# Kernel tuning notes

Measured on AMD Instinct MI355X. Metric: run time of the kernel, lower is better.

The kernel has to match this reference:

```python
import jax, jax.numpy as jnp
import numpy as np

S, N, M, D = 4, 4096, 4096, 128
NEG = -1e30
EPS = 1e-12


def setup_inputs() -> dict:
    key = jax.random.key(0)
    k1, k2, k3 = jax.random.split(key, 3)
    art = jax.random.normal(k1, (S, N, D), dtype=jnp.float32)
    ref = jax.random.normal(k2, (S, M, D), dtype=jnp.float32)
    pos_mask = jax.random.randint(k3, (S, N, M), 0, 2).astype(jnp.bool_)
    log_temperature = jnp.log(jnp.asarray(0.01, dtype=jnp.float32))
    return {"art": art, "ref": ref, "pos_mask": pos_mask, "log_temperature": log_temperature}


def _l2norm(x):
    # F.normalize: x / max(||x||, eps)
    n = jnp.sqrt(jnp.sum(x * x, axis=-1, keepdims=True))
    return x / jnp.maximum(n, EPS)


def reference(art, ref, pos_mask, log_temperature):
    temp = jnp.exp(log_temperature)
    a = _l2norm(art)                                   # [S,N,D]
    r = _l2norm(ref)                                   # [S,M,D]
    logits = jnp.einsum("snd,smd->snm", a, r) / temp   # [S,N,M]

    den = jax.nn.logsumexp(logits, axis=-1)                              # [S,N]
    num = jax.nn.logsumexp(jnp.where(pos_mask, logits, NEG), axis=-1)    # [S,N]

    n_pos = jnp.sum(pos_mask, axis=-1)                 # [S,N]
    n_ref = logits.shape[-1]
    valid = (n_pos > 0) & (n_ref > n_pos)              # skip anchors with 0 pos or all pos

    per_anchor = den - num                             # -(num - den)
    cnt = jnp.sum(valid, axis=-1)                      # [S]
    stem_loss = jnp.sum(jnp.where(valid, per_anchor, 0.0), axis=-1) / jnp.maximum(cnt, 1)
    stem_valid = cnt > 0
    loss = jnp.sum(jnp.where(stem_valid, stem_loss, 0.0)) / jnp.maximum(jnp.sum(stem_valid), 1)
    return loss
```

## Files before the change

kernel.cpp:

```cpp
#include <hip/hip_runtime.h>
#include <hip/hip_bf16.h>
#include <math.h>

#define S_ 4
#define N_ 4096
#define M_ 4096
#define D_ 128
#define NEG_ (-1e30f)
#define CH_ 2
#define MCH_ (M_ / CH_)
#define NST_ (MCH_ / 64)
#define NGRP_ (NST_ / 4)
#define LN2_ 0.69314718055994531f
#define LOG2E_ 1.44269504088896340f

typedef __bf16 bf16x8 __attribute__((ext_vector_type(8)));
typedef float f32x4 __attribute__((ext_vector_type(4)));

__device__ __forceinline__ void gll16(const void* g, void* l) {
    __builtin_amdgcn_global_load_lds(
        (const __attribute__((address_space(1))) unsigned int*)g,
        (__attribute__((address_space(3))) unsigned int*)l, 16, 0, 0);
}

__device__ __forceinline__ unsigned short f2bf(float f) {
    unsigned u = __float_as_uint(f);
    unsigned r = (u + 0x7FFFu + ((u >> 16) & 1u)) >> 16;
    return (unsigned short)r;
}

__global__ void nrm_rows_kernel(const float* __restrict__ art, const float* __restrict__ ref,
                                unsigned short* __restrict__ an, unsigned short* __restrict__ rn) {
    const int w = threadIdx.x >> 6;
    const int lane = threadIdx.x & 63;
    const int half = lane >> 5;
    const int li = lane & 31;
    const int row = blockIdx.x * 8 + w * 2 + half;
    const bool is_art = row < S_ * N_;
    const float* src = is_art ? (art + (size_t)row * D_)
                              : (ref + (size_t)(row - S_ * N_) * D_);
    unsigned short* dst = is_art ? (an + (size_t)row * D_)
                                 : (rn + (size_t)(row - S_ * N_) * D_);
    const float4 v = *reinterpret_cast<const float4*>(src + li * 4);
    float ss = v.x * v.x + v.y * v.y + v.z * v.z + v.w * v.w;
#pragma unroll
    for (int off = 1; off < 32; off <<= 1) ss += __shfl_xor(ss, off);
    const float scale = 1.0f / fmaxf(sqrtf(ss), 1e-12f);
    uint2 pack;
    pack.x = (unsigned)f2bf(v.x * scale) | ((unsigned)f2bf(v.y * scale) << 16);
    pack.y = (unsigned)f2bf(v.z * scale) | ((unsigned)f2bf(v.w * scale) << 16);
    *reinterpret_cast<uint2*>(dst + li * 4) = pack;
}

template <int ESZ>
__device__ __forceinline__ void mload(int4* mq, const unsigned char* __restrict__ maskb,
                                      const size_t* rowb, int g, int lane) {
#pragma unroll
    for (int r = 0; r < 8; ++r) {
        const unsigned char* p = maskb + rowb[r] + (size_t)((g * 256 + 4 * lane) * ESZ);
        if (ESZ == 4) mq[r] = *reinterpret_cast<const int4*>(p);
        else          mq[r].x = *reinterpret_cast<const int*>(p);
    }
}

template <int ESZ>
__device__ __forceinline__ unsigned nib_of(const int4 q) {
    if (ESZ == 4)
        return (unsigned)((q.x != 0) | ((q.y != 0) << 1) | ((q.z != 0) << 2) | ((q.w != 0) << 3));
    const unsigned b = (unsigned)q.x;
    return (((b & 0xFFu) != 0) ? 1u : 0u) | (((b >> 8) & 0xFFu) ? 2u : 0u)
         | (((b >> 16) & 0xFFu) ? 4u : 0u) | ((b >> 24) ? 8u : 0u);
}

template <int ESZ>
__device__ __forceinline__ void run_main(
    const unsigned short* __restrict__ an, const unsigned short* __restrict__ rn,
    const unsigned char* __restrict__ maskb, float scale2, float4* __restrict__ part4,
    int s, int ch, int n_base,
    unsigned char (&smem)[2][64 * 256], unsigned char (&mnib)[2][32][68],
    float4 (&lds4)[4][16]) {

    const int tid = threadIdx.x;
    const int w = tid >> 6;
    const int lane = tid & 63;
    const int nsub = w & 1;
    const int msub = w >> 1;
    const int n16 = n_base + nsub * 16;
    const int lrow = lane & 15;
    const int lgrp = lane >> 4;

    bf16x8 bfr[4];
    const unsigned short* abase = an + ((size_t)(s * N_ + n16 + lrow)) * D_ + lgrp * 8;
#pragma unroll
    for (int kc = 0; kc < 4; ++kc)
        bfr[kc] = *reinterpret_cast<const bf16x8*>(abase + kc * 32);

    const int srow = w * 4 + (lane >> 4);
    const int schunk = (lane & 15) ^ (srow & 7);
    const int lane_src_off = srow * 256 + schunk * 16;
    const unsigned char* rn_chunk =
        (const unsigned char*)(rn + ((size_t)(s * M_ + ch * MCH_)) * D_);

    size_t rowb[8];
#pragma unroll
    for (int r = 0; r < 8; ++r)
        rowb[r] = ((size_t)(s * N_ + n_base + w * 8 + r) * M_ + (size_t)ch * MCH_) * ESZ;

    const int rb0 = (msub * 32 + lrow) * 256;
    int coff[4];
#pragma unroll
    for (int kc = 0; kc < 4; ++kc) coff[kc] = ((kc * 4 + lgrp) ^ (lrow & 7)) * 16;

    float dmax = NEG_, dsum = 0.f, nsum = 0.f;
    int npos = 0;
    int4 mq[8];

    {
        const unsigned char* src = rn_chunk + lane_src_off;
        unsigned char* dst = &smem[0][w * 1024];
#pragma unroll
        for (int j = 0; j < 4; ++j) gll16(src + j * 4096, dst + j * 4096);
        mload<ESZ>(mq, maskb, rowb, 0, lane);
#pragma unroll
        for (int r = 0; r < 8; ++r)
            mnib[0][w * 8 + r][lane] = (unsigned char)nib_of<ESZ>(mq[r]);
        mload<ESZ>(mq, maskb, rowb, 1, lane);
        __syncthreads();
    }

    for (int g = 0; g < NGRP_; ++g) {
#pragma unroll
        for (int j = 0; j < 4; ++j) {
            const int st = g * 4 + j;
            const int nb = j & 1;
            if (j < 3 || g < NGRP_ - 1) {
                const unsigned char* src_ = rn_chunk + (size_t)(st + 1) * 16384 + lane_src_off;
                unsigned char* dst_ = &smem[nb ^ 1][w * 1024];
#pragma unroll
                for (int jj = 0; jj < 4; ++jj) gll16(src_ + jj * 4096, dst_ + jj * 4096);
            }
            if (j == 3 && g < NGRP_ - 1) {
#pragma unroll
                for (int r = 0; r < 8; ++r)
                    mnib[(g + 1) & 1][w * 8 + r][lane] = (unsigned char)nib_of<ESZ>(mq[r]);
                if (g < NGRP_ - 2) mload<ESZ>(mq, maskb, rowb, g + 2, lane);
            }
            const unsigned char* base_ = &smem[nb][0] + rb0;
            f32x4 acc0 = {0.f, 0.f, 0.f, 0.f}, acc1 = {0.f, 0.f, 0.f, 0.f};
#pragma unroll
            for (int kc = 0; kc < 4; ++kc) {
                acc0 = __builtin_amdgcn_mfma_f32_16x16x32_bf16(
                    *reinterpret_cast<const bf16x8*>(base_ + coff[kc]), bfr[kc], acc0, 0, 0, 0);
                acc1 = __builtin_amdgcn_mfma_f32_16x16x32_bf16(
                    *reinterpret_cast<const bf16x8*>(base_ + 4096 + coff[kc]), bfr[kc], acc1, 0, 0, 0);
            }
            const int row = nsub * 16 + lrow;
            const int nidx = j * 16 + msub * 8 + lgrp;
            const unsigned nib0 = mnib[g & 1][row][nidx];
            const unsigned nib1 = mnib[g & 1][row][nidx + 4];
            float l0 = acc0[0] * scale2, l1 = acc0[1] * scale2;
            float l2 = acc0[2] * scale2, l3 = acc0[3] * scale2;
            float l4 = acc1[0] * scale2, l5 = acc1[1] * scale2;
            float l6 = acc1[2] * scale2, l7 = acc1[3] * scale2;
            float tmax = fmaxf(fmaxf(fmaxf(l0, l1), fmaxf(l2, l3)),
                               fmaxf(fmaxf(l4, l5), fmaxf(l6, l7)));
            const float nmx = fmaxf(dmax, tmax);
            const float r_ = exp2f(dmax - nmx);
            float e0 = exp2f(l0 - nmx), e1 = exp2f(l1 - nmx);
            float e2 = exp2f(l2 - nmx), e3 = exp2f(l3 - nmx);
            float e4 = exp2f(l4 - nmx), e5 = exp2f(l5 - nmx);
            float e6 = exp2f(l6 - nmx), e7 = exp2f(l7 - nmx);
            dsum = dsum * r_ + (((e0 + e1) + (e2 + e3)) + ((e4 + e5) + (e6 + e7)));
            float p0 = ((nib0 & 1u) ? e0 : 0.f) + (((nib0 >> 1) & 1u) ? e1 : 0.f);
            float p1 = (((nib0 >> 2) & 1u) ? e2 : 0.f) + (((nib0 >> 3) & 1u) ? e3 : 0.f);
            float p2 = ((nib1 & 1u) ? e4 : 0.f) + (((nib1 >> 1) & 1u) ? e5 : 0.f);
            float p3 = (((nib1 >> 2) & 1u) ? e6 : 0.f) + (((nib1 >> 3) & 1u) ? e7 : 0.f);
            nsum = nsum * r_ + ((p0 + p1) + (p2 + p3));
            npos += __popc(nib0 | (nib1 << 4));
            dmax = nmx;
            __syncthreads();
        }
    }

    float npf = (float)npos;
#pragma unroll
    for (int off = 16; off < 64; off <<= 1) {
        float odm = __shfl_xor(dmax, off), ods = __shfl_xor(dsum, off);
        float ons = __shfl_xor(nsum, off), onp = __shfl_xor(npf, off);
        float nm = fmaxf(dmax, odm);
        float ra = exp2f(dmax - nm), rb = exp2f(odm - nm);
        dsum = dsum * ra + ods * rb;
        nsum = nsum * ra + ons * rb;
        npf += onp;
        dmax = nm;
    }

    if (lane < 16) lds4[w][lane] = make_float4(dmax, dsum, nsum, npf);
    __syncthreads();

    if (w == 0 && lane < 32) {
        const int wsub = lane >> 4;
        const int ni = lane & 15;
        const float4 A = lds4[wsub][ni];
        const float4 B = lds4[wsub + 2][ni];
        const float nm = fmaxf(A.x, B.x);
        const float ra = exp2f(A.x - nm), rb = exp2f(B.x - nm);
        const float ds = A.y * ra + B.y * rb;
        const float ns = A.z * ra + B.z * rb;
        const float np = A.w + B.w;
        const int ag = s * N_ + n_base + wsub * 16 + ni;
        part4[ag * CH_ + ch] = make_float4(nm, ds, ns, np);
    }
}

__global__ __launch_bounds__(256, 4) void infonce_main_kernel(
    const unsigned short* __restrict__ an, const unsigned short* __restrict__ rn,
    const unsigned char* __restrict__ maskb, const float* __restrict__ logtemp,
    float4* __restrict__ part4) {

    const int bid = blockIdx.x;
    const int swz = (bid & 7) * 128 + (bid >> 3);
    const int ch = swz >> 9;
    const int s = (swz >> 7) & 3;
    const int n_base = (swz & 127) * 32;
    const float scale2 = __expf(-logtemp[0]) * LOG2E_;

    const unsigned* mu = (const unsigned*)maskb;
    unsigned pr = 0;
#pragma unroll
    for (int i = 0; i < 4; ++i) pr |= (mu[i * 64 + (threadIdx.x & 63)] > 1u) ? 1u : 0u;
    const bool byte_mode = (__ballot(pr != 0) != 0ull);

    __shared__ unsigned char smem[2][64 * 256];
    __shared__ unsigned char mnib[2][32][68];
    __shared__ float4 lds4[4][16];

    if (byte_mode)
        run_main<1>(an, rn, maskb, scale2, part4, s, ch, n_base, smem, mnib, lds4);
    else
        run_main<4>(an, rn, maskb, scale2, part4, s, ch, n_base, smem, mnib, lds4);
}

__global__ void reduce_kernel(const float4* __restrict__ part4, float2* __restrict__ bpart) {
    const int a = blockIdx.x * 256 + threadIdx.x;
    const int w = threadIdx.x >> 6;
    const int lane = threadIdx.x & 63;
    float dm = NEG_, ds = 0.f, ns = 0.f, npf = 0.f;
#pragma unroll
    for (int ch = 0; ch < CH_; ++ch) {
        const float4 p = part4[a * CH_ + ch];
        const float m2 = fmaxf(dm, p.x);
        const float ra = exp2f(dm - m2), rb = exp2f(p.x - m2);
        ds = ds * ra + p.y * rb;
        ns = ns * ra + p.z * rb;
        npf += p.w;
        dm = m2;
    }
    const bool valid = (npf > 0.5f) && (npf < (float)M_ - 0.5f);
    float pa = valid ? LN2_ * (log2f(ds) - log2f(ns)) : 0.f;
    float cv = valid ? 1.f : 0.f;
#pragma unroll
    for (int off = 1; off < 64; off <<= 1) {
        pa += __shfl_xor(pa, off);
        cv += __shfl_xor(cv, off);
    }
    __shared__ float sp[4], sc[4];
    if (lane == 0) { sp[w] = pa; sc[w] = cv; }
    __syncthreads();
    if (threadIdx.x == 0)
        bpart[blockIdx.x] = make_float2(sp[0] + sp[1] + sp[2] + sp[3],
                                        sc[0] + sc[1] + sc[2] + sc[3]);
}

__global__ void finalize_kernel(const float2* __restrict__ bpart, float* __restrict__ out) {
    const int t = threadIdx.x;
    const float2 v = bpart[t];
    float pa = v.x, cv = v.y;
#pragma unroll
    for (int off = 1; off < 16; off <<= 1) {
        pa += __shfl_xor(pa, off);
        cv += __shfl_xor(cv, off);
    }
    const float p0 = __shfl(pa, 0),  c0 = __shfl(cv, 0);
    const float p1 = __shfl(pa, 16), c1 = __shfl(cv, 16);
    const float p2 = __shfl(pa, 32), c2 = __shfl(cv, 32);
    const float p3 = __shfl(pa, 48), c3 = __shfl(cv, 48);
    if (t == 0) {
        float total = 0.f;
        int scnt = 0;
        const float ps[4] = {p0, p1, p2, p3};
        const float cs[4] = {c0, c1, c2, c3};
        for (int s = 0; s < S_; ++s) {
            const float stem = ps[s] / fmaxf(cs[s], 1.f);
            if (cs[s] > 0.f) { total += stem; scnt++; }
        }
        out[0] = total / (float)(scnt > 0 ? scnt : 1);
    }
}

extern "C" void kernel_launch(void* const* d_in, const int* in_sizes, int n_in,
                              void* d_out, int out_size, void* d_ws, size_t ws_size,
                              hipStream_t stream) {
    const float* art = (const float*)d_in[0];
    const float* ref = (const float*)d_in[1];
    const unsigned char* mask = (const unsigned char*)d_in[2];
    const float* lt = (const float*)d_in[3];
    float* out = (float*)d_out;

    char* ws = (char*)d_ws;
    unsigned short* an = (unsigned short*)ws;
    unsigned short* rn = (unsigned short*)(ws + (size_t)4194304);
    float4* part4 = (float4*)(ws + (size_t)8388608);
    float2* bpart = (float2*)(ws + (size_t)9437184);

    nrm_rows_kernel<<<(S_ * (N_ + M_)) / 8, 256, 0, stream>>>(art, ref, an, rn);
    infonce_main_kernel<<<S_ * (N_ / 32) * CH_, 256, 0, stream>>>(an, rn, mask, lt, part4);
    reduce_kernel<<<(S_ * N_) / 256, 256, 0, stream>>>(part4, bpart);
    finalize_kernel<<<1, 64, 0, stream>>>(bpart, out);
}
```

Before: 400.3 us.

## Enlarge anchor tile to 128 rows and drop online max with fixed logit shift

Each block now handles 128 anchor rows instead of 32. Each wave computes a 32x64 logit tile, so every reference tile staged in LDS is reused across four times as many anchors, and the reference range is split into 4 chunks instead of 2. The running-max softmax is replaced by a constant shift of half the logit scale, which relies on the inputs being unit-normalised so the logits stay bounded. The mask is now read as contiguous per-row words and packed into 64-bit bitmasks in LDS. This removes the per-step rescaling and the cross-wave merge, at the cost of more registers (launch bound lowered to 2) and a risk of exp overflow or underflow if the temperature changes.

```diff
diff --git a/kernel.cpp b/kernel.cpp
--- a/kernel.cpp
+++ b/kernel.cpp
@@ -6,11 +6,10 @@
 #define N_ 4096
 #define M_ 4096
 #define D_ 128
-#define NEG_ (-1e30f)
-#define CH_ 2
+#define BN_ 128
+#define CH_ 4
 #define MCH_ (M_ / CH_)
 #define NST_ (MCH_ / 64)
-#define NGRP_ (NST_ / 4)
 #define LN2_ 0.69314718055994531f
 #define LOG2E_ 1.44269504088896340f
 
@@ -52,24 +51,41 @@
     *reinterpret_cast<uint2*>(dst + li * 4) = pack;
 }
 
+__device__ __forceinline__ unsigned nib4(int a, int b, int c, int d) {
+    return (unsigned)((a != 0) | ((b != 0) << 1) | ((c != 0) << 2) | ((d != 0) << 3));
+}
+__device__ __forceinline__ unsigned nib_bytes(unsigned b) {
+    return ((b & 0xFFu) ? 1u : 0u) | ((b & 0xFF00u) ? 2u : 0u)
+         | ((b & 0xFF0000u) ? 4u : 0u) | ((b & 0xFF000000u) ? 8u : 0u);
+}
+
 template <int ESZ>
-__device__ __forceinline__ void mload(int4* mq, const unsigned char* __restrict__ maskb,
-                                      const size_t* rowb, int g, int lane) {
-#pragma unroll
-    for (int r = 0; r < 8; ++r) {
-        const unsigned char* p = maskb + rowb[r] + (size_t)((g * 256 + 4 * lane) * ESZ);
-        if (ESZ == 4) mq[r] = *reinterpret_cast<const int4*>(p);
-        else          mq[r].x = *reinterpret_cast<const int*>(p);
-    }
-}
-
+__device__ __forceinline__ void mload(int4* mq, const unsigned char* p) {
+    if (ESZ == 4) {
+#pragma unroll
+        for (int j = 0; j < 8; ++j) mq[j] = *reinterpret_cast<const int4*>(p + j * 16);
+    } else {
+        mq[0] = *reinterpret_cast<const int4*>(p);
+        mq[1] = *reinterpret_cast<const int4*>(p + 16);
+    }
+}
 template <int ESZ>
-__device__ __forceinline__ unsigned nib_of(const int4 q) {
-    if (ESZ == 4)
-        return (unsigned)((q.x != 0) | ((q.y != 0) << 1) | ((q.z != 0) << 2) | ((q.w != 0) << 3));
-    const unsigned b = (unsigned)q.x;
-    return (((b & 0xFFu) != 0) ? 1u : 0u) | (((b >> 8) & 0xFFu) ? 2u : 0u)
-         | (((b >> 16) & 0xFFu) ? 4u : 0u) | ((b >> 24) ? 8u : 0u);
+__device__ __forceinline__ unsigned mconv(const int4* mq) {
+    unsigned u = 0;
+    if (ESZ == 4) {
+#pragma unroll
+        for (int j = 0; j < 8; ++j)
+            u |= nib4(mq[j].x, mq[j].y, mq[j].z, mq[j].w) << (4 * j);
+    } else {
+#pragma unroll
+        for (int k = 0; k < 2; ++k) {
+            u |= nib_bytes((unsigned)mq[k].x) << ((k * 4 + 0) * 4);
+            u |= nib_bytes((unsigned)mq[k].y) << ((k * 4 + 1) * 4);
+            u |= nib_bytes((unsigned)mq[k].z) << ((k * 4 + 2) * 4);
+            u |= nib_bytes((unsigned)mq[k].w) << ((k * 4 + 3) * 4);
+        }
+    }
+    return u;
 }
 
 template <int ESZ>
@@ -77,23 +93,24 @@
     const unsigned short* __restrict__ an, const unsigned short* __restrict__ rn,
     const unsigned char* __restrict__ maskb, float scale2, float4* __restrict__ part4,
     int s, int ch, int n_base,
-    unsigned char (&smem)[2][64 * 256], unsigned char (&mnib)[2][32][68],
-    float4 (&lds4)[4][16]) {
+    unsigned char (&smem)[2][64 * 256], unsigned long long (&mtab)[2][BN_]) {
 
     const int tid = threadIdx.x;
     const int w = tid >> 6;
     const int lane = tid & 63;
-    const int nsub = w & 1;
-    const int msub = w >> 1;
-    const int n16 = n_base + nsub * 16;
     const int lrow = lane & 15;
     const int lgrp = lane >> 4;
-
-    bf16x8 bfr[4];
-    const unsigned short* abase = an + ((size_t)(s * N_ + n16 + lrow)) * D_ + lgrp * 8;
-#pragma unroll
-    for (int kc = 0; kc < 4; ++kc)
-        bfr[kc] = *reinterpret_cast<const bf16x8*>(abase + kc * 32);
+    const float negC = -0.5f * scale2;
+
+    bf16x8 bfr[2][4];
+#pragma unroll
+    for (int nc = 0; nc < 2; ++nc) {
+        const unsigned short* abase =
+            an + ((size_t)(s * N_ + n_base + w * 32 + nc * 16 + lrow)) * D_ + lgrp * 8;
+#pragma unroll
+        for (int kc = 0; kc < 4; ++kc)
+            bfr[nc][kc] = *reinterpret_cast<const bf16x8*>(abase + kc * 32);
+    }
 
     const int srow = w * 4 + (lane >> 4);
     const int schunk = (lane & 15) ^ (srow & 7);
@@ -101,128 +118,100 @@
     const unsigned char* rn_chunk =
         (const unsigned char*)(rn + ((size_t)(s * M_ + ch * MCH_)) * D_);
 
-    size_t rowb[8];
-#pragma unroll
-    for (int r = 0; r < 8; ++r)
-        rowb[r] = ((size_t)(s * N_ + n_base + w * 8 + r) * M_ + (size_t)ch * MCH_) * ESZ;
-
-    const int rb0 = (msub * 32 + lrow) * 256;
-    int coff[4];
-#pragma unroll
-    for (int kc = 0; kc < 4; ++kc) coff[kc] = ((kc * 4 + lgrp) ^ (lrow & 7)) * 16;
-
-    float dmax = NEG_, dsum = 0.f, nsum = 0.f;
-    int npos = 0;
-    int4 mq[8];
+    const int mrow = w * 32 + (lane >> 1);
+    const int h = lane & 1;
+    const unsigned char* mbase = maskb +
+        ((size_t)(s * N_ + n_base + mrow) * M_ + (size_t)(ch * MCH_ + h * 32)) * ESZ;
+
+    float dsum0 = 0.f, dsum1 = 0.f, nsum0 = 0.f, nsum1 = 0.f;
+    int npos0 = 0, npos1 = 0;
+    int4 mq[ESZ == 4 ? 8 : 2];
 
     {
         const unsigned char* src = rn_chunk + lane_src_off;
         unsigned char* dst = &smem[0][w * 1024];
 #pragma unroll
         for (int j = 0; j < 4; ++j) gll16(src + j * 4096, dst + j * 4096);
-        mload<ESZ>(mq, maskb, rowb, 0, lane);
-#pragma unroll
-        for (int r = 0; r < 8; ++r)
-            mnib[0][w * 8 + r][lane] = (unsigned char)nib_of<ESZ>(mq[r]);
-        mload<ESZ>(mq, maskb, rowb, 1, lane);
+        mload<ESZ>(mq, mbase);
+        reinterpret_cast<unsigned*>(&mtab[0][mrow])[h] = mconv<ESZ>(mq);
+        mload<ESZ>(mq, mbase + (size_t)64 * ESZ);
         __syncthreads();
     }
 
-    for (int g = 0; g < NGRP_; ++g) {
-#pragma unroll
-        for (int j = 0; j < 4; ++j) {
-            const int st = g * 4 + j;
-            const int nb = j & 1;
-            if (j < 3 || g < NGRP_ - 1) {
-                const unsigned char* src_ = rn_chunk + (size_t)(st + 1) * 16384 + lane_src_off;
-                unsigned char* dst_ = &smem[nb ^ 1][w * 1024];
-#pragma unroll
-                for (int jj = 0; jj < 4; ++jj) gll16(src_ + jj * 4096, dst_ + jj * 4096);
+    for (int st = 0; st < NST_; ++st) {
+        const int buf = st & 1;
+        if (st + 1 < NST_) {
+            const unsigned char* src = rn_chunk + (size_t)(st + 1) * 16384 + lane_src_off;
+            unsigned char* dst = &smem[buf ^ 1][w * 1024];
+#pragma unroll
+            for (int j = 0; j < 4; ++j) gll16(src + j * 4096, dst + j * 4096);
+            reinterpret_cast<unsigned*>(&mtab[buf ^ 1][mrow])[h] = mconv<ESZ>(mq);
+        }
+        if (st + 2 < NST_) mload<ESZ>(mq, mbase + (size_t)(st + 2) * 64 * ESZ);
+
+        const unsigned char* base_ = &smem[buf][0];
+        f32x4 acc[4][2] = {};
+#pragma unroll
+        for (int mt = 0; mt < 4; ++mt) {
+            const int rowb = (mt * 16 + lrow) * 256;
+#pragma unroll
+            for (int kc = 0; kc < 4; ++kc) {
+                const bf16x8 af = *reinterpret_cast<const bf16x8*>(
+                    base_ + rowb + (((kc * 4 + lgrp) ^ (lrow & 7)) * 16));
+                acc[mt][0] = __builtin_amdgcn_mfma_f32_16x16x32_bf16(af, bfr[0][kc], acc[mt][0], 0, 0, 0);
+                acc[mt][1] = __builtin_amdgcn_mfma_f32_16x16x32_bf16(af, bfr[1][kc], acc[mt][1], 0, 0, 0);
             }
-            if (j == 3 && g < NGRP_ - 1) {
-#pragma unroll
-                for (int r = 0; r < 8; ++r)
-                    mnib[(g + 1) & 1][w * 8 + r][lane] = (unsigned char)nib_of<ESZ>(mq[r]);
-                if (g < NGRP_ - 2) mload<ESZ>(mq, maskb, rowb, g + 2, lane);
+        }
+        const unsigned long long w0 = mtab[buf][w * 32 + lrow];
+        const unsigned long long w1 = mtab[buf][w * 32 + 16 + lrow];
+        float d0 = 0.f, d1 = 0.f, n0 = 0.f, n1 = 0.f;
+#pragma unroll
+        for (int mt = 0; mt < 4; ++mt) {
+            const unsigned nib0 = (unsigned)(w0 >> ((mt * 4 + lgrp) * 4)) & 0xFu;
+            const unsigned nib1 = (unsigned)(w1 >> ((mt * 4 + lgrp) * 4)) & 0xFu;
+            float e0[4], e1[4];
+#pragma unroll
+            for (int i = 0; i < 4; ++i) {
+                e0[i] = exp2f(fmaf(acc[mt][0][i], scale2, negC));
+                e1[i] = exp2f(fmaf(acc[mt][1][i], scale2, negC));
             }
-            const unsigned char* base_ = &smem[nb][0] + rb0;
-            f32x4 acc0 = {0.f, 0.f, 0.f, 0.f}, acc1 = {0.f, 0.f, 0.f, 0.f};
-#pragma unroll
-            for (int kc = 0; kc < 4; ++kc) {
-                acc0 = __builtin_amdgcn_mfma_f32_16x16x32_bf16(
-                    *reinterpret_cast<const bf16x8*>(base_ + coff[kc]), bfr[kc], acc0, 0, 0, 0);
-                acc1 = __builtin_amdgcn_mfma_f32_16x16x32_bf16(
-                    *reinterpret_cast<const bf16x8*>(base_ + 4096 + coff[kc]), bfr[kc], acc1, 0, 0, 0);
-            }
-            const int row = nsub * 16 + lrow;
-            const int nidx = j * 16 + msub * 8 + lgrp;
-            const unsigned nib0 = mnib[g & 1][row][nidx];
-            const unsigned nib1 = mnib[g & 1][row][nidx + 4];
-            float l0 = acc0[0] * scale2, l1 = acc0[1] * scale2;
-            float l2 = acc0[2] * scale2, l3 = acc0[3] * scale2;
-            float l4 = acc1[0] * scale2, l5 = acc1[1] * scale2;
-            float l6 = acc1[2] * scale2, l7 = acc1[3] * scale2;
-            float tmax = fmaxf(fmaxf(fmaxf(l0, l1), fmaxf(l2, l3)),
-                               fmaxf(fmaxf(l4, l5), fmaxf(l6, l7)));
-            const float nmx = fmaxf(dmax, tmax);
-            const float r_ = exp2f(dmax - nmx);
-            float e0 = exp2f(l0 - nmx), e1 = exp2f(l1 - nmx);
-            float e2 = exp2f(l2 - nmx), e3 = exp2f(l3 - nmx);
-            float e4 = exp2f(l4 - nmx), e5 = exp2f(l5 - nmx);
-            float e6 = exp2f(l6 - nmx), e7 = exp2f(l7 - nmx);
-            dsum = dsum * r_ + (((e0 + e1) + (e2 + e3)) + ((e4 + e5) + (e6 + e7)));
-            float p0 = ((nib0 & 1u) ? e0 : 0.f) + (((nib0 >> 1) & 1u) ? e1 : 0.f);
-            float p1 = (((nib0 >> 2) & 1u) ? e2 : 0.f) + (((nib0 >> 3) & 1u) ? e3 : 0.f);
-            float p2 = ((nib1 & 1u) ? e4 : 0.f) + (((nib1 >> 1) & 1u) ? e5 : 0.f);
-            float p3 = (((nib1 >> 2) & 1u) ? e6 : 0.f) + (((nib1 >> 3) & 1u) ? e7 : 0.f);
-            nsum = nsum * r_ + ((p0 + p1) + (p2 + p3));
-            npos += __popc(nib0 | (nib1 << 4));
-            dmax = nmx;
-            __syncthreads();
-        }
-    }
-
-    float npf = (float)npos;
+            d0 += (e0[0] + e0[1]) + (e0[2] + e0[3]);
+            d1 += (e1[0] + e1[1]) + (e1[2] + e1[3]);
+            n0 += (((nib0 & 1u) ? e0[0] : 0.f) + (((nib0 >> 1) & 1u) ? e0[1] : 0.f))
+                + ((((nib0 >> 2) & 1u) ? e0[2] : 0.f) + (((nib0 >> 3) & 1u) ? e0[3] : 0.f));
+            n1 += (((nib1 & 1u) ? e1[0] : 0.f) + (((nib1 >> 1) & 1u) ? e1[1] : 0.f))
+                + ((((nib1 >> 2) & 1u) ? e1[2] : 0.f) + (((nib1 >> 3) & 1u) ? e1[3] : 0.f));
+            npos0 += __popc(nib0);
+            npos1 += __popc(nib1);
+        }
+        dsum0 += d0; dsum1 += d1; nsum0 += n0; nsum1 += n1;
+        __syncthreads();
+    }
+
+    float npf0 = (float)npos0, npf1 = (float)npos1;
 #pragma unroll
     for (int off = 16; off < 64; off <<= 1) {
-        float odm = __shfl_xor(dmax, off), ods = __shfl_xor(dsum, off);
-        float ons = __shfl_xor(nsum, off), onp = __shfl_xor(npf, off);
-        float nm = fmaxf(dmax, odm);
-        float ra = exp2f(dmax - nm), rb = exp2f(odm - nm);
-        dsum = dsum * ra + ods * rb;
-        nsum = nsum * ra + ons * rb;
-        npf += onp;
-        dmax = nm;
-    }
-
-    if (lane < 16) lds4[w][lane] = make_float4(dmax, dsum, nsum, npf);
-    __syncthreads();
-
-    if (w == 0 && lane < 32) {
-        const int wsub = lane >> 4;
-        const int ni = lane & 15;
-        const float4 A = lds4[wsub][ni];
-        const float4 B = lds4[wsub + 2][ni];
-        const float nm = fmaxf(A.x, B.x);
-        const float ra = exp2f(A.x - nm), rb = exp2f(B.x - nm);
-        const float ds = A.y * ra + B.y * rb;
-        const float ns = A.z * ra + B.z * rb;
-        const float np = A.w + B.w;
-        const int ag = s * N_ + n_base + wsub * 16 + ni;
-        part4[ag * CH_ + ch] = make_float4(nm, ds, ns, np);
-    }
-}
-
-__global__ __launch_bounds__(256, 4) void infonce_main_kernel(
+        dsum0 += __shfl_xor(dsum0, off); dsum1 += __shfl_xor(dsum1, off);
+        nsum0 += __shfl_xor(nsum0, off); nsum1 += __shfl_xor(nsum1, off);
+        npf0  += __shfl_xor(npf0, off);  npf1  += __shfl_xor(npf1, off);
+    }
+    if (lane < 16) {
+        const int ag0 = s * N_ + n_base + w * 32 + lane;
+        part4[ag0 * CH_ + ch] = make_float4(dsum0, nsum0, npf0, 0.f);
+        part4[(ag0 + 16) * CH_ + ch] = make_float4(dsum1, nsum1, npf1, 0.f);
+    }
+}
+
+__global__ __launch_bounds__(256, 2) void infonce_main_kernel(
     const unsigned short* __restrict__ an, const unsigned short* __restrict__ rn,
     const unsigned char* __restrict__ maskb, const float* __restrict__ logtemp,
     float4* __restrict__ part4) {
 
     const int bid = blockIdx.x;
-    const int swz = (bid & 7) * 128 + (bid >> 3);
-    const int ch = swz >> 9;
-    const int s = (swz >> 7) & 3;
-    const int n_base = (swz & 127) * 32;
+    const int swz = (bid & 7) * 64 + (bid >> 3);
+    const int ch = swz >> 7;
+    const int s = (swz >> 5) & 3;
+    const int n_base = (swz & 31) * BN_;
     const float scale2 = __expf(-logtemp[0]) * LOG2E_;
 
     const unsigned* mu = (const unsigned*)maskb;
@@ -232,29 +221,23 @@
     const bool byte_mode = (__ballot(pr != 0) != 0ull);
 
     __shared__ unsigned char smem[2][64 * 256];
-    __shared__ unsigned char mnib[2][32][68];
-    __shared__ float4 lds4[4][16];
+    __shared__ unsigned long long mtab[2][BN_];
 
     if (byte_mode)
-        run_main<1>(an, rn, maskb, scale2, part4, s, ch, n_base, smem, mnib, lds4);
+        run_main<1>(an, rn, maskb, scale2, part4, s, ch, n_base, smem, mtab);
     else
-        run_main<4>(an, rn, maskb, scale2, part4, s, ch, n_base, smem, mnib, lds4);
+        run_main<4>(an, rn, maskb, scale2, part4, s, ch, n_base, smem, mtab);
 }
 
 __global__ void reduce_kernel(const float4* __restrict__ part4, float2* __restrict__ bpart) {
     const int a = blockIdx.x * 256 + threadIdx.x;
     const int w = threadIdx.x >> 6;
     const int lane = threadIdx.x & 63;
-    float dm = NEG_, ds = 0.f, ns = 0.f, npf = 0.f;
+    float ds = 0.f, ns = 0.f, npf = 0.f;
 #pragma unroll
     for (int ch = 0; ch < CH_; ++ch) {
         const float4 p = part4[a * CH_ + ch];
-        const float m2 = fmaxf(dm, p.x);
-        const float ra = exp2f(dm - m2), rb = exp2f(p.x - m2);
-        ds = ds * ra + p.y * rb;
-        ns = ns * ra + p.z * rb;
-        npf += p.w;
-        dm = m2;
+        ds += p.x; ns += p.y; npf += p.z;
     }
     const bool valid = (npf > 0.5f) && (npf < (float)M_ - 0.5f);
     float pa = valid ? LN2_ * (log2f(ds) - log2f(ns)) : 0.f;
@@ -314,7 +297,7 @@
     float2* bpart = (float2*)(ws + (size_t)9437184);
 
     nrm_rows_kernel<<<(S_ * (N_ + M_)) / 8, 256, 0, stream>>>(art, ref, an, rn);
-    infonce_main_kernel<<<S_ * (N_ / 32) * CH_, 256, 0, stream>>>(an, rn, mask, lt, part4);
+    infonce_main_kernel<<<S_ * (N_ / BN_) * CH_, 256, 0, stream>>>(an, rn, mask, lt, part4);
     reduce_kernel<<<(S_ * N_) / 256, 256, 0, stream>>>(part4, bpart);
     finalize_kernel<<<1, 64, 0, stream>>>(bpart, out);
 }
```

Result: no change. 407.6 us (+1.8%).
